# Kernel tuning notes

Measured on AMD Instinct MI355X. Metric: run time of the kernel, lower is better.

The kernel has to match this reference:

```python
import jax, jax.numpy as jnp
import numpy as np

N_EMBD = 768
N_HEAD = 12
HEAD_DIM = N_EMBD // N_HEAD


def setup_inputs() -> dict:
    key = jax.random.key(0)
    k1, k2, k3 = jax.random.split(key, 3)
    B, T, C = 4, 2048, N_EMBD
    x = jax.random.normal(k1, (B, T, C), dtype=jnp.float32)
    # c_attn: torch Linear(C, 3C) -> store as (C, 3C) for x @ W
    w_attn = jax.random.normal(k2, (C, 3 * C), dtype=jnp.float32) * (1.0 / np.sqrt(C))
    b_attn = jax.random.normal(k3, (3 * C,), dtype=jnp.float32) * 0.02
    return {"x": x, "w_attn": w_attn, "b_attn": b_attn}


def reference(x, w_attn, b_attn):
    B, T, C = x.shape
    H, D = N_HEAD, HEAD_DIM
    scale = 1.0 / np.sqrt(D).astype(np.float32)

    qkv = x @ w_attn + b_attn                      # (B, T, 3C)
    q, k, v = jnp.split(qkv, 3, axis=-1)
    q = q.reshape(B, T, H, D).transpose(0, 2, 1, 3)  # (B, H, T, D)
    k = k.reshape(B, T, H, D).transpose(0, 2, 1, 3)
    v = v.reshape(B, T, H, D).transpose(0, 2, 1, 3)

    att = jnp.einsum('bhid,bhjd->bhij', q, k) * scale  # (B, H, T, T)
    causal = jnp.tril(jnp.ones((T, T), dtype=bool))
    # masked positions -> -inf -> relu -> 0; kept positions -> relu(scaled score)
    att = jnp.where(causal, jnp.maximum(att, 0.0), 0.0)

    y = jnp.einsum('bhij,bhjd->bhid', att, v)      # (B, H, T, D)
    y = y.transpose(0, 2, 1, 3).reshape(B, T, C)
    return y
```

## Files before the change

kernel.cpp:

```cpp
#include <hip/hip_runtime.h>
#include <hip/hip_bf16.h>

typedef short bf16x8 __attribute__((ext_vector_type(8)));
typedef float f32x4  __attribute__((ext_vector_type(4)));
typedef unsigned short u16x4 __attribute__((ext_vector_type(4)));

#define CDIM   768
#define NQKV   2304
#define MROWS  8192
#define TSEQ   2048
#define HD     64
#define NHEAD  12
#define BHTOT  48

__device__ __forceinline__ unsigned short f2bf(float f) {
    unsigned int x;
    __builtin_memcpy(&x, &f, 4);
    unsigned int r = (x + 0x7fffu + ((x >> 16) & 1u)) >> 16;
    return (unsigned short)r;
}

__device__ __forceinline__ unsigned int pkbf(float a, float b) {
    unsigned int ua, ub;
    __builtin_memcpy(&ua, &a, 4);
    __builtin_memcpy(&ub, &b, 4);
    return __builtin_amdgcn_perm(ua + 0x8000u, ub + 0x8000u, 0x03020706u);
}

__device__ __forceinline__ f32x4 mfma16(bf16x8 a, bf16x8 b, f32x4 c) {
    return __builtin_amdgcn_mfma_f32_16x16x32_bf16(a, b, c, 0, 0, 0);
}

__device__ __forceinline__ void gl_lds16(const unsigned short* g, unsigned short* l) {
    __builtin_amdgcn_global_load_lds(
        (__attribute__((address_space(1))) void*)(g),
        (__attribute__((address_space(3))) void*)(l),
        16, 0, 0);
}

__global__ __launch_bounds__(256) void convert_x(
    const float* __restrict__ X, unsigned short* __restrict__ Xb)
{
    size_t i = ((size_t)blockIdx.x * 256 + threadIdx.x) * 4;
    f32x4 v = *(const f32x4*)(X + i);
    u16x4 o;
#pragma unroll
    for (int j = 0; j < 4; j++) o[j] = f2bf(v[j]);
    *(u16x4*)(Xb + i) = o;
}

__global__ __launch_bounds__(256) void transpose_w(
    const float* __restrict__ W, unsigned short* __restrict__ Wt)
{
    __shared__ __align__(16) unsigned short tile[64][72];
    const int bx = blockIdx.x;
    const int by = blockIdx.y;
    const int tid = threadIdx.x;
#pragma unroll
    for (int c = 0; c < 4; c++) {
        int chunk = tid + 256 * c;
        int r = chunk >> 4, cc = chunk & 15;
        f32x4 v = *(const f32x4*)(W + (size_t)(by * 64 + r) * NQKV + bx * 64 + cc * 4);
#pragma unroll
        for (int j = 0; j < 4; j++) tile[cc * 4 + j][r] = f2bf(v[j]);
    }
    __syncthreads();
#pragma unroll
    for (int c = 0; c < 2; c++) {
        int chunk = tid + 256 * c;
        int r = chunk >> 3, cc = chunk & 7;
        bf16x8 v;
#pragma unroll
        for (int j = 0; j < 8; j++) v[j] = (short)tile[r][cc * 8 + j];
        *(bf16x8*)(Wt + (size_t)(bx * 64 + r) * CDIM + by * 64 + cc * 8) = v;
    }
}

#define BM 128
#define BN 128
#define BK 64

__global__ __launch_bounds__(256, 4) void qkv_gemm(
    const unsigned short* __restrict__ X,
    const unsigned short* __restrict__ Wt,
    const float* __restrict__ Bias,
    unsigned short* __restrict__ Q,
    unsigned short* __restrict__ Km,
    unsigned short* __restrict__ Vt)
{
    __shared__ __align__(16) unsigned short As[BM * BK];
    __shared__ __align__(16) unsigned short Bs[BN * BK];
    const int tid  = threadIdx.x;
    const int wave = tid >> 6, lane = tid & 63;
    const int quad = lane >> 4, m16 = lane & 15;
    const int wr = wave >> 1, wc = wave & 1;
    const int m0 = blockIdx.y * BM, n0 = blockIdx.x * BN;

    f32x4 acc[4][4];
#pragma unroll
    for (int i = 0; i < 4; i++)
#pragma unroll
        for (int j = 0; j < 4; j++) acc[i][j] = f32x4{0.f, 0.f, 0.f, 0.f};

    const unsigned short* xb = X + (size_t)m0 * CDIM;
    const unsigned short* wb = Wt + (size_t)n0 * CDIM;

    const int srow[4] = {
        (wave * 256 + 0 * 64 + lane) >> 3, (wave * 256 + 1 * 64 + lane) >> 3,
        (wave * 256 + 2 * 64 + lane) >> 3, (wave * 256 + 3 * 64 + lane) >> 3 };
    const int spos = lane & 7;

    const int rb = m16 & 7;

    for (int k0 = 0; k0 < CDIM; k0 += BK) {
#pragma unroll
        for (int c = 0; c < 4; c++) {
            int row = srow[c];
            int ch = spos ^ (row & 7);
            gl_lds16(xb + (size_t)row * CDIM + k0 + ch * 8, As + wave * 2048 + c * 512);
            gl_lds16(wb + (size_t)row * CDIM + k0 + ch * 8, Bs + wave * 2048 + c * 512);
        }
        __syncthreads();
#pragma unroll
        for (int ks = 0; ks < 2; ks++) {
            bf16x8 af[4], bfg[4];
#pragma unroll
            for (int t = 0; t < 4; t++) {
                int rowa = wr * 64 + t * 16 + m16;
                int rowb = wc * 64 + t * 16 + m16;
                int pos = (ks * 4 + quad) ^ rb;
                af[t]  = *(const bf16x8*)(As + rowa * 64 + pos * 8);
                bfg[t] = *(const bf16x8*)(Bs + rowb * 64 + pos * 8);
            }
#pragma unroll
            for (int i = 0; i < 4; i++)
#pragma unroll
                for (int j = 0; j < 4; j++)
                    acc[i][j] = mfma16(af[i], bfg[j], acc[i][j]);
        }
        __syncthreads();
    }

    const int region = n0 / CDIM;
    const float qscale = (region == 0) ? 0.125f : 1.0f;
#pragma unroll
    for (int i = 0; i < 4; i++) {
        int row = m0 + wr * 64 + i * 16 + quad * 4;
#pragma unroll
        for (int j = 0; j < 4; j++) {
            int gcol = n0 + wc * 64 + j * 16 + m16;
            int cc = gcol - region * CDIM;
            int h = cc >> 6, d = cc & 63;
            float bv = Bias[gcol];
#pragma unroll
            for (int r = 0; r < 4; r++) {
                int gm = row + r;
                int b = gm >> 11, t = gm & 2047;
                int bh = b * NHEAD + h;
                unsigned short o = f2bf((acc[i][j][r] + bv) * qscale);
                if (region == 0)      Q[((size_t)bh * TSEQ + t) * HD + d] = o;
                else if (region == 1) Km[((size_t)bh * TSEQ + t) * HD + d] = o;
                else                  Vt[((size_t)bh * HD + d) * TSEQ + t] = o;
            }
        }
    }
}

#define LDSK 0
#define LDSV 8192

__global__ __launch_bounds__(256, 4) void attn(
    const unsigned short* __restrict__ Q,
    const unsigned short* __restrict__ Kmat,
    const unsigned short* __restrict__ Vt,
    float* __restrict__ Out)
{
    __shared__ __align__(16) unsigned short S[16384];

    const int tid  = threadIdx.x;
    const int wave = tid >> 6, lane = tid & 63;
    const int q4 = lane >> 4, m16 = lane & 15;
    const int q8 = m16 >> 2, m3 = m16 & 3;
    const int par = (m3 ^ (m3 >> 1)) & 1;

    const int bh = blockIdx.x >> 4;
    const int it = 15 - (blockIdx.x & 15);
    const int i0 = it * 128;

    const unsigned short* qb = Q    + (size_t)bh * TSEQ * HD;
    const unsigned short* kb = Kmat + (size_t)bh * TSEQ * HD;
    const unsigned short* vb = Vt   + (size_t)bh * HD * TSEQ;

    bf16x8 qf[2][2];
#pragma unroll
    for (int si = 0; si < 2; si++)
#pragma unroll
        for (int ks = 0; ks < 2; ks++)
            qf[si][ks] = *(const bf16x8*)(qb +
                (size_t)(i0 + wave * 32 + si * 16 + m16) * HD + ks * 32 + q4 * 8);

    f32x4 oacc[2][4];
#pragma unroll
    for (int si = 0; si < 2; si++)
#pragma unroll
        for (int dn = 0; dn < 4; dn++) oacc[si][dn] = f32x4{0.f, 0.f, 0.f, 0.f};

    const int kbase0 = q8 * 512 + m3 * 64 + q4 * 8 + par * 32;
    const int kbase1 = q8 * 512 + m3 * 64 + q4 * 8 + 32 - par * 32;
    const int vbase0 = m16 * 128 + q4 * 8 + par * 32;
    const int vbase1 = m16 * 128 + q4 * 8 + 32 - par * 32;

    for (int jt = 0; jt <= it; jt++) {
        const int j0 = jt * 128;
#pragma unroll
        for (int cc = 0; cc < 4; cc++) {
            int cs = wave * 4 + cc;
            {
                int s = cs * 64 + lane;
                int row = s >> 3, ch = s & 7;
                int c = ch ^ (((row ^ (row >> 1)) & 1) * 4);
                gl_lds16(kb + (size_t)(j0 + row) * HD + c * 8, &S[LDSK] + cs * 512);
            }
            {
                int s = cs * 64 + lane;
                int d = s >> 4, ch = s & 15;
                int c = ch ^ (((d ^ (d >> 1)) & 1) * 4);
                gl_lds16(vb + (size_t)d * TSEQ + j0 + c * 8, &S[LDSV] + cs * 512);
            }
        }
        __syncthreads();

        const bool diag = (jt == it);
#pragma unroll
        for (int kk = 0; kk < 4; kk++) {
            bf16x8 kf_e0 = *(const bf16x8*)(&S[LDSK] + kbase0 + kk * 2048);
            bf16x8 kf_e1 = *(const bf16x8*)(&S[LDSK] + kbase1 + kk * 2048);
            bf16x8 kf_o0 = *(const bf16x8*)(&S[LDSK] + kbase0 + kk * 2048 + 256);
            bf16x8 kf_o1 = *(const bf16x8*)(&S[LDSK] + kbase1 + kk * 2048 + 256);

            f32x4 sacc[2][2];
#pragma unroll
            for (int o = 0; o < 2; o++)
#pragma unroll
                for (int si = 0; si < 2; si++) sacc[o][si] = f32x4{0.f, 0.f, 0.f, 0.f};
#pragma unroll
            for (int si = 0; si < 2; si++) {
                sacc[0][si] = mfma16(kf_e0, qf[si][0], sacc[0][si]);
                sacc[0][si] = mfma16(kf_e1, qf[si][1], sacc[0][si]);
                sacc[1][si] = mfma16(kf_o0, qf[si][0], sacc[1][si]);
                sacc[1][si] = mfma16(kf_o1, qf[si][1], sacc[1][si]);
            }

            unsigned int pk[2][2][2];
#pragma unroll
            for (int o = 0; o < 2; o++)
#pragma unroll
                for (int si = 0; si < 2; si++) {
                    f32x4 v = sacc[o][si];
                    if (diag) {
#pragma unroll
                        for (int r = 0; r < 4; r++) {
                            int gj = kk * 32 + q4 * 8 + o * 4 + r;
                            int gi = wave * 32 + si * 16 + m16;
                            if (gj > gi) v[r] = 0.f;
                        }
                    }
#pragma unroll
                    for (int r = 0; r < 4; r++) v[r] = fmaxf(v[r], 0.f);
                    pk[o][si][0] = pkbf(v[0], v[1]);
                    pk[o][si][1] = pkbf(v[2], v[3]);
                }

#pragma unroll
            for (int dn = 0; dn < 4; dn++) {
                const int vb_off = ((kk & 1) ? vbase1 : vbase0) + (kk >> 1) * 64 + dn * 2048;
                bf16x8 vf = *(const bf16x8*)(&S[LDSV] + vb_off);
#pragma unroll
                for (int si = 0; si < 2; si++) {
                    union { bf16x8 v; unsigned int u[4]; } af;
                    af.u[0] = pk[0][si][0];
                    af.u[1] = pk[0][si][1];
                    af.u[2] = pk[1][si][0];
                    af.u[3] = pk[1][si][1];
                    oacc[si][dn] = mfma16(af.v, vf, oacc[si][dn]);
                }
            }
        }
        __syncthreads();
    }

    const int b = bh / NHEAD, h = bh % NHEAD;
#pragma unroll
    for (int si = 0; si < 2; si++) {
        int ri = i0 + wave * 32 + si * 16 + q4 * 4;
#pragma unroll
        for (int dn = 0; dn < 4; dn++) {
            int d = dn * 16 + m16;
#pragma unroll
            for (int r = 0; r < 4; r++) {
                Out[((size_t)b * TSEQ + ri + r) * CDIM + h * HD + d] = oacc[si][dn][r];
            }
        }
    }
}

extern "C" void kernel_launch(void* const* d_in, const int* in_sizes, int n_in,
                              void* d_out, int out_size, void* d_ws, size_t ws_size,
                              hipStream_t stream) {
    const float* X    = (const float*)d_in[0];
    const float* W    = (const float*)d_in[1];
    const float* Bias = (const float*)d_in[2];
    float* out = (float*)d_out;

    unsigned short* Xb = (unsigned short*)d_ws;
    unsigned short* Wt = Xb + (size_t)MROWS * CDIM;
    unsigned short* Q  = Wt + (size_t)NQKV * CDIM;
    unsigned short* Km = Q  + (size_t)BHTOT * TSEQ * HD;
    unsigned short* Vt = Km + (size_t)BHTOT * TSEQ * HD;

    hipLaunchKernelGGL(convert_x, dim3((MROWS * CDIM) / 1024), dim3(256), 0, stream, X, Xb);
    hipLaunchKernelGGL(transpose_w, dim3(NQKV / 64, CDIM / 64), dim3(256), 0, stream, W, Wt);
    hipLaunchKernelGGL(qkv_gemm, dim3(NQKV / BN, MROWS / BM), dim3(256), 0, stream,
                       Xb, Wt, Bias, Q, Km, Vt);
    hipLaunchKernelGGL(attn, dim3(BHTOT * 16), dim3(256), 0, stream, Q, Km, Vt, out);
}
```

Baseline: 194.2 us.

## Use full XOR swizzle for K/V LDS tiles and XCD-aware block mapping

Replaces the one-bit parity swizzle of the K and V shared-memory tiles with a wider XOR swizzle over 8 chunk positions, so that fragment reads from LDS hit fewer bank conflicts. It also remaps block indices so each XCD (blockIdx & 7) handles a fixed group of six batch-heads, which keeps K/V reuse inside one L2 slice. The costs are more index arithmetic and a different order of causal work across XCDs, which could change load balance.

```diff
diff --git a/kernel.cpp b/kernel.cpp
--- a/kernel.cpp
+++ b/kernel.cpp
@@ -109,7 +109,6 @@
         (wave * 256 + 0 * 64 + lane) >> 3, (wave * 256 + 1 * 64 + lane) >> 3,
         (wave * 256 + 2 * 64 + lane) >> 3, (wave * 256 + 3 * 64 + lane) >> 3 };
     const int spos = lane & 7;
-
     const int rb = m16 & 7;
 
     for (int k0 = 0; k0 < CDIM; k0 += BK) {
@@ -181,11 +180,12 @@
     const int wave = tid >> 6, lane = tid & 63;
     const int q4 = lane >> 4, m16 = lane & 15;
     const int q8 = m16 >> 2, m3 = m16 & 3;
-    const int par = (m3 ^ (m3 >> 1)) & 1;
-
-    const int bh = blockIdx.x >> 4;
-    const int it = 15 - (blockIdx.x & 15);
-    const int i0 = it * 128;
+
+    const int xcd = blockIdx.x & 7;
+    const int idx = blockIdx.x >> 3;
+    const int bh  = xcd * 6 + (idx % 6);
+    const int it  = 15 - (idx / 6);
+    const int i0  = it * 128;
 
     const unsigned short* qb = Q    + (size_t)bh * TSEQ * HD;
     const unsigned short* kb = Kmat + (size_t)bh * TSEQ * HD;
@@ -205,10 +205,10 @@
 #pragma unroll
         for (int dn = 0; dn < 4; dn++) oacc[si][dn] = f32x4{0.f, 0.f, 0.f, 0.f};
 
-    const int kbase0 = q8 * 512 + m3 * 64 + q4 * 8 + par * 32;
-    const int kbase1 = q8 * 512 + m3 * 64 + q4 * 8 + 32 - par * 32;
-    const int vbase0 = m16 * 128 + q4 * 8 + par * 32;
-    const int vbase1 = m16 * 128 + q4 * 8 + 32 - par * 32;
+    const int fr  = ((q8 & 1) << 2) | m3;
+    const int kx0 = (q4 ^ fr) * 8;
+    const int kx1 = kx0 ^ 32;
+    const int krb = (q8 * 8 + m3) * 64;
 
     for (int jt = 0; jt <= it; jt++) {
         const int j0 = jt * 128;
@@ -216,16 +216,14 @@
         for (int cc = 0; cc < 4; cc++) {
             int cs = wave * 4 + cc;
             {
-                int s = cs * 64 + lane;
-                int row = s >> 3, ch = s & 7;
-                int c = ch ^ (((row ^ (row >> 1)) & 1) * 4);
-                gl_lds16(kb + (size_t)(j0 + row) * HD + c * 8, &S[LDSK] + cs * 512);
+                int rowK = cs * 8 + (lane >> 3);
+                int chK  = (lane & 7) ^ ((((rowK >> 3) & 1) << 2) | (rowK & 3));
+                gl_lds16(kb + (size_t)(j0 + rowK) * HD + chK * 8, &S[LDSK] + cs * 512);
             }
             {
-                int s = cs * 64 + lane;
-                int d = s >> 4, ch = s & 15;
-                int c = ch ^ (((d ^ (d >> 1)) & 1) * 4);
-                gl_lds16(vb + (size_t)d * TSEQ + j0 + c * 8, &S[LDSV] + cs * 512);
+                int dV  = cs * 4 + (lane >> 4);
+                int chV = (m16 & 8) | ((m16 ^ dV) & 7);
+                gl_lds16(vb + (size_t)dV * TSEQ + j0 + chV * 8, &S[LDSV] + cs * 512);
             }
         }
         __syncthreads();
@@ -233,10 +231,11 @@
         const bool diag = (jt == it);
 #pragma unroll
         for (int kk = 0; kk < 4; kk++) {
-            bf16x8 kf_e0 = *(const bf16x8*)(&S[LDSK] + kbase0 + kk * 2048);
-            bf16x8 kf_e1 = *(const bf16x8*)(&S[LDSK] + kbase1 + kk * 2048);
-            bf16x8 kf_o0 = *(const bf16x8*)(&S[LDSK] + kbase0 + kk * 2048 + 256);
-            bf16x8 kf_o1 = *(const bf16x8*)(&S[LDSK] + kbase1 + kk * 2048 + 256);
+            const int kb0 = kk * 2048 + krb;
+            bf16x8 kf_e0 = *(const bf16x8*)(&S[LDSK] + kb0 + kx0);
+            bf16x8 kf_e1 = *(const bf16x8*)(&S[LDSK] + kb0 + kx1);
+            bf16x8 kf_o0 = *(const bf16x8*)(&S[LDSK] + kb0 + 256 + kx0);
+            bf16x8 kf_o1 = *(const bf16x8*)(&S[LDSK] + kb0 + 256 + kx1);
 
             f32x4 sacc[2][2];
 #pragma unroll
@@ -273,8 +272,8 @@
 
 #pragma unroll
             for (int dn = 0; dn < 4; dn++) {
-                const int vb_off = ((kk & 1) ? vbase1 : vbase0) + (kk >> 1) * 64 + dn * 2048;
-                bf16x8 vf = *(const bf16x8*)(&S[LDSV] + vb_off);
+                int vsw = ((kk * 4 + q4) ^ (m16 & 7)) * 8;
+                bf16x8 vf = *(const bf16x8*)(&S[LDSV] + (dn * 16 + m16) * 128 + vsw);
 #pragma unroll
                 for (int si = 0; si < 2; si++) {
                     union { bf16x8 v; unsigned int u[4]; } af;
```

Result: faster. 182.1 us (-6.2%).
